# Kernel tuning notes

Hardware: AMD Instinct MI355X
Metric: run time of the kernel (lower is better)

## Reference

```python
import jax, jax.numpy as jnp
import numpy as np

V, E, P, NL, H, I = 50304, 512, 320, 6, 8, 1024
B, S = 2, 1024
HD = P // H            # head_dim = 40
ROT = int(HD * 0.25)   # rotary dims = 10


def layer_norm(x, w, b, eps=1e-5):
    m = jnp.mean(x, -1, keepdims=True)
    v = jnp.mean((x - m) ** 2, -1, keepdims=True)
    return (x - m) * jax.lax.rsqrt(v + eps) * w + b


def setup_inputs() -> dict:
    key = jax.random.key(0)
    ks = jax.random.split(key, 16)
    n = lambda k, s: jax.random.normal(k, s, dtype=jnp.float32) * 0.02
    return dict(
        input_ids=jax.random.randint(ks[0], (B, S), 0, V),
        embed_w=n(ks[1], (V, E)),
        embed_norm_w=jnp.ones((E,)), embed_norm_b=jnp.zeros((E,)),
        dproj_w=n(ks[2], (P + E, P)), dproj_b=jnp.zeros((P,)),
        dproj_ln_w=jnp.ones((P,)), dproj_ln_b=jnp.zeros((P,)),
        ln1_w=jnp.ones((NL, P)), ln1_b=jnp.zeros((NL, P)),
        ln2_w=jnp.ones((NL, P)), ln2_b=jnp.zeros((NL, P)),
        qkv_w=n(ks[3], (NL, P, 3 * P)), qkv_b=jnp.zeros((NL, 3 * P)),
        dense_w=n(ks[4], (NL, P, P)), dense_b=jnp.zeros((NL, P)),
        fc1_w=n(ks[5], (NL, P, I)), fc1_b=jnp.zeros((NL, I)),
        fc2_w=n(ks[6], (NL, I, P)), fc2_b=jnp.zeros((NL, P)),
        final_ln_w=jnp.ones((P,)), final_ln_b=jnp.zeros((P,)),
        lm_head_w=n(ks[7], (V, P)),
    )


def _forward(input_ids, embed_w, embed_norm_w, embed_norm_b, dproj_w, dproj_b,
             dproj_ln_w, dproj_ln_b, ln1_w, ln1_b, ln2_w, ln2_b, qkv_w, qkv_b,
             dense_w, dense_b, fc1_w, fc1_b, fc2_w, fc2_b, final_ln_w, final_ln_b,
             lm_head_w):
    b, s = input_ids.shape
    # 1-2) token embedding + LayerNorm
    te = layer_norm(embed_w[input_ids], embed_norm_w, embed_norm_b)  # [B,S,E]

    # 3) sequential DiverseProjection recurrence over seq_len (lax.scan)
    def step(prev, emb_t):  # prev [B,P], emb_t [B,E]
        h = jnp.concatenate([prev, emb_t], -1) @ dproj_w + dproj_b
        h = jnp.tanh(layer_norm(h, dproj_ln_w, dproj_ln_b))
        return h, h
    _, hs = jax.lax.scan(step, jnp.zeros((b, P), te.dtype), jnp.swapaxes(te, 0, 1))
    x = jnp.swapaxes(hs, 0, 1)  # [B,S,P]

    # RoPE tables (GPT-NeoX style, rotary_pct = 0.25 of head_dim)
    half = ROT // 2
    inv = 1.0 / (10000.0 ** (jnp.arange(0, ROT, 2, dtype=jnp.float32) / ROT))
    freqs = jnp.arange(s, dtype=jnp.float32)[:, None] * inv[None, :]  # [S, ROT/2]
    cos = jnp.cos(jnp.concatenate([freqs, freqs], -1))  # [S, ROT]
    sin = jnp.sin(jnp.concatenate([freqs, freqs], -1))

    def rope(t):  # t: [B,H,S,ROT]
        t1, t2 = t[..., :half], t[..., half:]
        return t * cos + jnp.concatenate([-t2, t1], -1) * sin

    mask = jnp.tril(jnp.ones((s, s), dtype=bool))
    scale = 1.0 / np.sqrt(HD)
    # 4) Pythia (GPT-NeoX) layers: parallel residual attn + mlp
    for l in range(NL):
        a_in = layer_norm(x, ln1_w[l], ln1_b[l])
        qkv = (a_in @ qkv_w[l] + qkv_b[l]).reshape(b, s, H, 3 * HD)
        q, k, v = (jnp.swapaxes(t, 1, 2) for t in jnp.split(qkv, 3, axis=-1))  # [B,H,S,HD]
        q = jnp.concatenate([rope(q[..., :ROT]), q[..., ROT:]], -1)
        k = jnp.concatenate([rope(k[..., :ROT]), k[..., ROT:]], -1)
        scores = jnp.einsum('bhqd,bhkd->bhqk', q, k) * scale
        attn = jax.nn.softmax(jnp.where(mask, scores, jnp.float32(-1e9)), axis=-1)
        ctx = jnp.einsum('bhqk,bhkd->bhqd', attn, v)
        attn_out = jnp.swapaxes(ctx, 1, 2).reshape(b, s, P) @ dense_w[l] + dense_b[l]
        m_in = layer_norm(x, ln2_w[l], ln2_b[l])
        mlp_out = jax.nn.gelu(m_in @ fc1_w[l] + fc1_b[l]) @ fc2_w[l] + fc2_b[l]
        x = x + attn_out + mlp_out
    # 5-6) final LN + LM head (no bias)
    x = layer_norm(x, final_ln_w, final_ln_b)
    return x @ lm_head_w.T  # [B,S,V]


def reference(input_ids, embed_w, embed_norm_w, embed_norm_b, dproj_w, dproj_b,
              dproj_ln_w, dproj_ln_b, ln1_w, ln1_b, ln2_w, ln2_b, qkv_w, qkv_b,
              dense_w, dense_b, fc1_w, fc1_b, fc2_w, fc2_b, final_ln_w, final_ln_b,
              lm_head_w):
    return _forward(input_ids, embed_w, embed_norm_w, embed_norm_b, dproj_w, dproj_b,
                    dproj_ln_w, dproj_ln_b, ln1_w, ln1_b, ln2_w, ln2_b, qkv_w, qkv_b,
                    dense_w, dense_b, fc1_w, fc1_b, fc2_w, fc2_b, final_ln_w,
                    final_ln_b, lm_head_w)
```

## Files before the change

### kernel.cpp

```cpp
#include <hip/hip_runtime.h>

#define VV 50304
#define EE 512
#define PP 320
#define NL 6
#define NH 8
#define II 1024
#define BB 2
#define SS 1024
#define HDD 40

typedef __attribute__((ext_vector_type(8))) __bf16 bf16x8;
typedef __attribute__((ext_vector_type(4))) float f32x4;

__device__ __forceinline__ float gelu_tanh(float x) {
    float x3 = x * x * x;
    return 0.5f * x * (1.f + tanhf(0.7978845608028654f * (x + 0.044715f * x3)));
}

__global__ __launch_bounds__(64) void embed_ln_kernel(
    const int* __restrict__ ids, const float* __restrict__ embed,
    const float* __restrict__ w, const float* __restrict__ b, float* __restrict__ out)
{
    int r = blockIdx.x;
    int lane = threadIdx.x;
    long id = ids[r];
    const float* xr = embed + id * (long)EE;
    float vals[8];
    float s = 0.f;
#pragma unroll
    for (int i = 0; i < 8; ++i) { vals[i] = xr[lane + i * 64]; s += vals[i]; }
#pragma unroll
    for (int m = 32; m >= 1; m >>= 1) s += __shfl_xor(s, m);
    float mean = s * (1.f / 512.f);
    float v = 0.f;
#pragma unroll
    for (int i = 0; i < 8; ++i) { float d = vals[i] - mean; v += d * d; }
#pragma unroll
    for (int m = 32; m >= 1; m >>= 1) v += __shfl_xor(v, m);
    float rstd = rsqrtf(v * (1.f / 512.f) + 1e-5f);
    float* orow = out + (long)r * EE;
#pragma unroll
    for (int i = 0; i < 8; ++i) {
        int c = lane + i * 64;
        orow[c] = (vals[i] - mean) * rstd * w[c] + b[c];
    }
}

__global__ __launch_bounds__(64) void ln_kernel(
    const float* __restrict__ x, const float* __restrict__ w,
    const float* __restrict__ b, float* __restrict__ out, int N)
{
    int r = blockIdx.x, lane = threadIdx.x;
    const float* xr = x + (long)r * N;
    float s = 0.f;
    for (int i = lane; i < N; i += 64) s += xr[i];
#pragma unroll
    for (int m = 32; m >= 1; m >>= 1) s += __shfl_xor(s, m);
    float mean = s / (float)N;
    float v = 0.f;
    for (int i = lane; i < N; i += 64) { float d = xr[i] - mean; v += d * d; }
#pragma unroll
    for (int m = 32; m >= 1; m >>= 1) v += __shfl_xor(v, m);
    float rstd = rsqrtf(v / (float)N + 1e-5f);
    float* orow = out + (long)r * N;
    for (int i = lane; i < N; i += 64) orow[i] = (xr[i] - mean) * rstd * w[i] + b[i];
}

__global__ __launch_bounds__(256) void gemm_kernel(
    const float* __restrict__ A, const float* __restrict__ B,
    const float* __restrict__ bias, float* __restrict__ C,
    int M, int N, int K, int BT, int act,
    const float* __restrict__ add1, const float* __restrict__ add2)
{
    __shared__ __align__(16) __bf16 As[64 * 40];
    __shared__ __align__(16) __bf16 Bs[64 * 40];
    int tid  = threadIdx.x;
    int lane = tid & 63;
    int wv   = tid >> 6;
    int l15  = lane & 15, quad = lane >> 4;
    int bm = blockIdx.y * 64, bn = blockIdx.x * 64;
    int wm = (wv >> 1) * 32, wn = (wv & 1) * 32;
    f32x4 acc[2][2] = {};

    int sm = tid >> 2;
    int sk = (tid & 3) * 8;
    int bk_n = tid & 63;
    int bk_k = (tid >> 6) * 8;

    for (int k0 = 0; k0 < K; k0 += 32) {
        {
            const float* ap = A + (long)(bm + sm) * K + k0 + sk;
            float4 a0 = *(const float4*)ap;
            float4 a1 = *(const float4*)(ap + 4);
            bf16x8 av;
            av[0] = (__bf16)a0.x; av[1] = (__bf16)a0.y; av[2] = (__bf16)a0.z; av[3] = (__bf16)a0.w;
            av[4] = (__bf16)a1.x; av[5] = (__bf16)a1.y; av[6] = (__bf16)a1.z; av[7] = (__bf16)a1.w;
            *(bf16x8*)&As[sm * 40 + sk] = av;
        }
        if (BT == 0) {
            const float* bp = B + (long)(k0 + bk_k) * N + bn + bk_n;
            bf16x8 bv;
#pragma unroll
            for (int i = 0; i < 8; ++i) bv[i] = (__bf16)bp[(long)i * N];
            *(bf16x8*)&Bs[bk_n * 40 + bk_k] = bv;
        } else {
            const float* bp = B + (long)(bn + sm) * K + k0 + sk;
            float4 b0 = *(const float4*)bp;
            float4 b1 = *(const float4*)(bp + 4);
            bf16x8 bv;
            bv[0] = (__bf16)b0.x; bv[1] = (__bf16)b0.y; bv[2] = (__bf16)b0.z; bv[3] = (__bf16)b0.w;
            bv[4] = (__bf16)b1.x; bv[5] = (__bf16)b1.y; bv[6] = (__bf16)b1.z; bv[7] = (__bf16)b1.w;
            *(bf16x8*)&Bs[sm * 40 + sk] = bv;
        }
        __syncthreads();
#pragma unroll
        for (int mt = 0; mt < 2; ++mt) {
            bf16x8 af = *(const bf16x8*)&As[(wm + mt * 16 + l15) * 40 + quad * 8];
#pragma unroll
            for (int nt = 0; nt < 2; ++nt) {
                bf16x8 bfr = *(const bf16x8*)&Bs[(wn + nt * 16 + l15) * 40 + quad * 8];
                acc[mt][nt] = __builtin_amdgcn_mfma_f32_16x16x32_bf16(af, bfr, acc[mt][nt], 0, 0, 0);
            }
        }
        __syncthreads();
    }
#pragma unroll
    for (int mt = 0; mt < 2; ++mt)
#pragma unroll
    for (int nt = 0; nt < 2; ++nt)
#pragma unroll
    for (int r = 0; r < 4; ++r) {
        int grow = bm + wm + mt * 16 + quad * 4 + r;
        int gcol = bn + wn + nt * 16 + l15;
        float v = acc[mt][nt][r];
        if (bias) v += bias[gcol];
        if (act == 1) v = gelu_tanh(v);
        long idx = (long)grow * N + gcol;
        if (add1) v += add1[idx];
        if (add2) v += add2[idx];
        C[idx] = v;
    }
}

__global__ __launch_bounds__(640) void scan_kernel(
    const float* __restrict__ Wtop,
    const float* __restrict__ c,
    const float* __restrict__ lnw, const float* __restrict__ lnb,
    float* __restrict__ x)
{
    __shared__ __align__(16) __bf16 hA[16 * 328];
    __shared__ float yb[2][PP];
    __shared__ float red[24];

    int tid = threadIdx.x;
    int lane = tid & 63;
    int w = tid >> 6;
    int l15 = lane & 15, quad = lane >> 4;

    for (int i = tid; i < 16 * 328; i += 640) hA[i] = (__bf16)0.f;

    bf16x8 bw[2][10];
#pragma unroll
    for (int nt = 0; nt < 2; ++nt) {
        int nn = (w * 2 + nt) * 16 + l15;
#pragma unroll
        for (int kt = 0; kt < 10; ++kt) {
#pragma unroll
            for (int j = 0; j < 8; ++j) {
                int kk = kt * 32 + quad * 8 + j;
                bw[nt][kt][j] = (__bf16)Wtop[(long)kk * PP + nn];
            }
        }
    }

    int sb = tid / PP;
    int jj = tid % PP;
    float lw = lnw[jj], lb = lnb[jj];
    __syncthreads();

    for (int t = 0; t < SS; ++t) {
        float cv = c[((long)sb * SS + t) * PP + jj];
        f32x4 acc0 = {0.f, 0.f, 0.f, 0.f}, acc1 = {0.f, 0.f, 0.f, 0.f};
#pragma unroll
        for (int kt = 0; kt < 10; ++kt) {
            bf16x8 a = *(const bf16x8*)&hA[l15 * 328 + kt * 32 + quad * 8];
            acc0 = __builtin_amdgcn_mfma_f32_16x16x32_bf16(a, bw[0][kt], acc0, 0, 0, 0);
            acc1 = __builtin_amdgcn_mfma_f32_16x16x32_bf16(a, bw[1][kt], acc1, 0, 0, 0);
        }
        if (quad == 0) {
            yb[0][(w * 2 + 0) * 16 + l15] = acc0[0];
            yb[1][(w * 2 + 0) * 16 + l15] = acc0[1];
            yb[0][(w * 2 + 1) * 16 + l15] = acc1[0];
            yb[1][(w * 2 + 1) * 16 + l15] = acc1[1];
        }
        __syncthreads();
        float yv = yb[sb][jj] + cv;
        float s1 = yv, s2 = yv * yv;
#pragma unroll
        for (int m = 32; m >= 1; m >>= 1) { s1 += __shfl_xor(s1, m); s2 += __shfl_xor(s2, m); }
        if (lane == 0) { red[w * 2] = s1; red[w * 2 + 1] = s2; }
        __syncthreads();
        float S1 = 0.f, S2 = 0.f;
        int wbase = sb * 5;
#pragma unroll
        for (int i = 0; i < 5; ++i) { S1 += red[(wbase + i) * 2]; S2 += red[(wbase + i) * 2 + 1]; }
        float mean = S1 * (1.f / (float)PP);
        float var  = S2 * (1.f / (float)PP) - mean * mean;
        float h = tanhf((yv - mean) * rsqrtf(var + 1e-5f) * lw + lb);
        x[((long)sb * SS + t) * PP + jj] = h;
        hA[sb * 328 + jj] = (__bf16)h;
        __syncthreads();
    }
}

__global__ __launch_bounds__(256) void rope_kernel(float* __restrict__ qkv)
{
    int t = blockIdx.x * 256 + threadIdx.x;
    if (t >= BB * SS * NH) return;
    int h = t & 7;
    int s = (t >> 3) & (SS - 1);
    int b = t >> 13;
    float* p = qkv + ((long)(b * SS + s)) * 960 + h * 120;
    const float inv[5] = {1.f, 0.158489319f, 0.0251188643f, 0.00398107171f, 0.000630957344f};
    float* q = p;
    float* k = p + HDD;
#pragma unroll
    for (int i = 0; i < 5; ++i) {
        float ang = (float)s * inv[i];
        float sn, cs;
        sincosf(ang, &sn, &cs);
        float q1 = q[i], q2 = q[i + 5];
        q[i]     = q1 * cs - q2 * sn;
        q[i + 5] = q2 * cs + q1 * sn;
        float k1 = k[i], k2 = k[i + 5];
        k[i]     = k1 * cs - k2 * sn;
        k[i + 5] = k2 * cs + k1 * sn;
    }
}

__global__ __launch_bounds__(256) void attn_kernel(
    const float* __restrict__ qkv, float* __restrict__ ctx)
{
    int qt = blockIdx.x & 15;
    int h  = (blockIdx.x >> 4) & 7;
    int b  = blockIdx.x >> 7;
    int tid = threadIdx.x;
    __shared__ float Qs[64][41], Ks[64][41], Vs[64][41];
    __shared__ float Ss[64][65];
    __shared__ float mS[64], lS[64], aS[64];
    const float scale = 0.15811388300841897f;
    long base = (long)b * SS * 960 + h * 120;
    int q0 = qt * 64;

    for (int i = tid; i < 64 * HDD; i += 256) {
        int r = i / HDD, d = i % HDD;
        Qs[r][d] = qkv[base + (long)(q0 + r) * 960 + d] * scale;
    }
    if (tid < 64) { mS[tid] = -1e30f; lS[tid] = 0.f; }
    float O[10];
#pragma unroll
    for (int i = 0; i < 10; ++i) O[i] = 0.f;
    int qo = tid >> 2, dg = (tid & 3) * 10;
    int sq = tid >> 2, sk16 = (tid & 3) * 16;
    __syncthreads();

    for (int kt = 0; kt <= qt; ++kt) {
        int k0 = kt * 64;
        for (int i = tid; i < 64 * HDD; i += 256) {
            int r = i / HDD, d = i % HDD;
            Ks[r][d] = qkv[base + (long)(k0 + r) * 960 + HDD + d];
            Vs[r][d] = qkv[base + (long)(k0 + r) * 960 + 2 * HDD + d];
        }
        __syncthreads();
#pragma unroll 1
        for (int kk = 0; kk < 16; ++kk) {
            int kcol = sk16 + kk;
            float s = 0.f;
#pragma unroll
            for (int d = 0; d < HDD; ++d) s += Qs[sq][d] * Ks[kcol][d];
            if (k0 + kcol > q0 + sq) s = -1e9f;
            Ss[sq][kcol] = s;
        }
        __syncthreads();
        if (tid < 64) {
            float mOld = mS[tid];
            float mNew = mOld;
            for (int j = 0; j < 64; ++j) mNew = fmaxf(mNew, Ss[tid][j]);
            float alpha = __expf(mOld - mNew);
            float psum = 0.f;
            for (int j = 0; j < 64; ++j) {
                float p = __expf(Ss[tid][j] - mNew);
                Ss[tid][j] = p;
                psum += p;
            }
            lS[tid] = lS[tid] * alpha + psum;
            mS[tid] = mNew;
            aS[tid] = alpha;
        }
        __syncthreads();
        float alpha = aS[qo];
#pragma unroll
        for (int i = 0; i < 10; ++i) O[i] *= alpha;
        for (int k = 0; k < 64; ++k) {
            float p = Ss[qo][k];
#pragma unroll
            for (int i = 0; i < 10; ++i) O[i] += p * Vs[k][dg + i];
        }
        __syncthreads();
    }
    float linv = 1.f / lS[qo];
#pragma unroll
    for (int i = 0; i < 10; ++i)
        ctx[((long)(b * SS + q0 + qo)) * PP + h * HDD + dg + i] = O[i] * linv;
}

extern "C" void kernel_launch(void* const* d_in, const int* in_sizes, int n_in,
                              void* d_out, int out_size, void* d_ws, size_t ws_size,
                              hipStream_t stream)
{
    (void)in_sizes; (void)n_in; (void)out_size; (void)ws_size;
    const int*   ids       = (const int*)d_in[0];
    const float* embed_w   = (const float*)d_in[1];
    const float* embed_nw  = (const float*)d_in[2];
    const float* embed_nb  = (const float*)d_in[3];
    const float* dproj_w   = (const float*)d_in[4];
    const float* dproj_b   = (const float*)d_in[5];
    const float* dproj_lnw = (const float*)d_in[6];
    const float* dproj_lnb = (const float*)d_in[7];
    const float* ln1_w     = (const float*)d_in[8];
    const float* ln1_b     = (const float*)d_in[9];
    const float* ln2_w     = (const float*)d_in[10];
    const float* ln2_b     = (const float*)d_in[11];
    const float* qkv_w     = (const float*)d_in[12];
    const float* qkv_b     = (const float*)d_in[13];
    const float* dense_w   = (const float*)d_in[14];
    const float* dense_b   = (const float*)d_in[15];
    const float* fc1_w     = (const float*)d_in[16];
    const float* fc1_b     = (const float*)d_in[17];
    const float* fc2_w     = (const float*)d_in[18];
    const float* fc2_b     = (const float*)d_in[19];
    const float* fln_w     = (const float*)d_in[20];
    const float* fln_b     = (const float*)d_in[21];
    const float* lm_w      = (const float*)d_in[22];
    float* out = (float*)d_out;
    float* ws  = (float*)d_ws;

    const long R = (long)BB * SS;
    float* te    = ws;
    float* cbuf  = te   + 1048576;
    float* x     = cbuf + 655360;
    float* lnbuf = x    + 655360;
    float* qkv   = lnbuf + 655360;
    float* ctx   = qkv  + 1966080;
    float* attn  = ctx  + 655360;
    float* mlp1  = attn + 655360;

    embed_ln_kernel<<<R, 64, 0, stream>>>(ids, embed_w, embed_nw, embed_nb, te);
    gemm_kernel<<<dim3(PP / 64, R / 64), 256, 0, stream>>>(
        te, dproj_w + (long)PP * PP, dproj_b, cbuf, R, PP, EE, 0, 0, nullptr, nullptr);
    scan_kernel<<<1, 640, 0, stream>>>(dproj_w, cbuf, dproj_lnw, dproj_lnb, x);

    for (int l = 0; l < NL; ++l) {
        ln_kernel<<<R, 64, 0, stream>>>(x, ln1_w + l * PP, ln1_b + l * PP, lnbuf, PP);
        gemm_kernel<<<dim3(960 / 64, R / 64), 256, 0, stream>>>(
            lnbuf, qkv_w + (long)l * PP * 960, qkv_b + l * 960, qkv, R, 960, PP, 0, 0, nullptr, nullptr);
        rope_kernel<<<(BB * SS * NH + 255) / 256, 256, 0, stream>>>(qkv);
        attn_kernel<<<BB * NH * 16, 256, 0, stream>>>(qkv, ctx);
        gemm_kernel<<<dim3(PP / 64, R / 64), 256, 0, stream>>>(
            ctx, dense_w + (long)l * PP * PP, dense_b + l * PP, attn, R, PP, PP, 0, 0, nullptr, nullptr);
        ln_kernel<<<R, 64, 0, stream>>>(x, ln2_w + l * PP, ln2_b + l * PP, lnbuf, PP);
        gemm_kernel<<<dim3(II / 64, R / 64), 256, 0, stream>>>(
            lnbuf, fc1_w + (long)l * PP * II, fc1_b + l * II, mlp1, R, II, PP, 0, 1, nullptr, nullptr);
        gemm_kernel<<<dim3(PP / 64, R / 64), 256, 0, stream>>>(
            mlp1, fc2_w + (long)l * II * PP, fc2_b + l * PP, x, R, PP, II, 0, 0, x, attn);
    }
    ln_kernel<<<R, 64, 0, stream>>>(x, fln_w, fln_b, lnbuf, PP);
    gemm_kernel<<<dim3(VV / 64, R / 64), 256, 0, stream>>>(
        lnbuf, lm_w, nullptr, out, R, VV, PP, 1, 0, nullptr, nullptr);
}
```

Before: 4.395 ms.

## Restructure sequential scan kernel to 4 waves with DPP reductions and prefetch

Rewrites the sequential projection scan so one block of 4 waves runs it instead of 10, and each wave computes 5 column tiles with MFMA. The per-row LayerNorm statistics are reduced with DPP within 16-lane groups and combined across waves through a small shared array, removing one of the three barriers per timestep. The next step's c values are prefetched into registers, and tanhf is replaced by an exp-based formula with clamping. Fewer waves mean fewer MFMAs in parallel per step and more register pressure from holding 50 weight fragments per lane.

```diff
diff --git a/kernel.cpp b/kernel.cpp
--- a/kernel.cpp
+++ b/kernel.cpp
@@ -17,6 +17,18 @@
     float x3 = x * x * x;
     return 0.5f * x * (1.f + tanhf(0.7978845608028654f * (x + 0.044715f * x3)));
 }
+
+template<int CTRL>
+__device__ __forceinline__ float dpp_reduce_add(float v) {
+    int s = __builtin_amdgcn_update_dpp(0, __builtin_bit_cast(int, v), CTRL, 0xF, 0xF, true);
+    return v + __builtin_bit_cast(float, s);
+}
+#define DPPRED16(x) do { \
+    x = dpp_reduce_add<0xB1>(x);   \
+    x = dpp_reduce_add<0x4E>(x);   \
+    x = dpp_reduce_add<0x141>(x);  \
+    x = dpp_reduce_add<0x140>(x);  \
+} while (0)
 
 __global__ __launch_bounds__(64) void embed_ln_kernel(
     const int* __restrict__ ids, const float* __restrict__ embed,
@@ -143,27 +155,27 @@
     }
 }
 
-__global__ __launch_bounds__(640) void scan_kernel(
+__global__ __launch_bounds__(256, 1) void scan_kernel(
     const float* __restrict__ Wtop,
     const float* __restrict__ c,
     const float* __restrict__ lnw, const float* __restrict__ lnb,
     float* __restrict__ x)
 {
     __shared__ __align__(16) __bf16 hA[16 * 328];
-    __shared__ float yb[2][PP];
-    __shared__ float red[24];
+    __shared__ __align__(16) float yb2[PP * 2];
+    __shared__ __align__(16) float red[16];
 
     int tid = threadIdx.x;
     int lane = tid & 63;
     int w = tid >> 6;
     int l15 = lane & 15, quad = lane >> 4;
 
-    for (int i = tid; i < 16 * 328; i += 640) hA[i] = (__bf16)0.f;
-
-    bf16x8 bw[2][10];
-#pragma unroll
-    for (int nt = 0; nt < 2; ++nt) {
-        int nn = (w * 2 + nt) * 16 + l15;
+    for (int i = tid; i < 16 * 328; i += 256) hA[i] = (__bf16)0.f;
+
+    bf16x8 bw[5][10];
+#pragma unroll
+    for (int nt = 0; nt < 5; ++nt) {
+        int nn = w * 80 + nt * 16 + l15;
 #pragma unroll
         for (int kt = 0; kt < 10; ++kt) {
 #pragma unroll
@@ -174,42 +186,98 @@
         }
     }
 
-    int sb = tid / PP;
-    int jj = tid % PP;
-    float lw = lnw[jj], lb = lnb[jj];
+    int nv = (tid < 128) ? 3 : 2;
+    int vb[3], vcol[3];
+    vb[0] = 0;            vcol[0] = tid;
+    vb[1] = (tid >= 64);  vcol[1] = vb[1] ? (tid - 64) : (tid + 256);
+    vb[2] = 1;            vcol[2] = tid + 192;
+    float lwv[3], lbv[3];
+    long xbase[3]; int ybo[3], hao[3];
+#pragma unroll
+    for (int i = 0; i < 3; ++i) {
+        if (i < nv) {
+            lwv[i] = lnw[vcol[i]]; lbv[i] = lnb[vcol[i]];
+            xbase[i] = (long)vb[i] * SS * PP + vcol[i];
+            ybo[i] = vcol[i] * 2 + vb[i];
+            hao[i] = vb[i] * 328 + vcol[i];
+        }
+    }
+
+    int ccol = w * 80 + l15;
+    const float* cp0 = c + ccol;
+    const float* cp1 = c + (long)SS * PP + ccol;
+    float cc0[5], cc1[5];
+#pragma unroll
+    for (int nt = 0; nt < 5; ++nt) { cc0[nt] = cp0[nt * 16]; cc1[nt] = cp1[nt * 16]; }
     __syncthreads();
 
     for (int t = 0; t < SS; ++t) {
-        float cv = c[((long)sb * SS + t) * PP + jj];
-        f32x4 acc0 = {0.f, 0.f, 0.f, 0.f}, acc1 = {0.f, 0.f, 0.f, 0.f};
+        int tn = (t + 1 < SS) ? (t + 1) : t;
+        float nc0[5], nc1[5];
+#pragma unroll
+        for (int nt = 0; nt < 5; ++nt) {
+            nc0[nt] = cp0[(long)tn * PP + nt * 16];
+            nc1[nt] = cp1[(long)tn * PP + nt * 16];
+        }
+
+        f32x4 acc[5] = {};
 #pragma unroll
         for (int kt = 0; kt < 10; ++kt) {
             bf16x8 a = *(const bf16x8*)&hA[l15 * 328 + kt * 32 + quad * 8];
-            acc0 = __builtin_amdgcn_mfma_f32_16x16x32_bf16(a, bw[0][kt], acc0, 0, 0, 0);
-            acc1 = __builtin_amdgcn_mfma_f32_16x16x32_bf16(a, bw[1][kt], acc1, 0, 0, 0);
-        }
+#pragma unroll
+            for (int nt = 0; nt < 5; ++nt)
+                acc[nt] = __builtin_amdgcn_mfma_f32_16x16x32_bf16(a, bw[nt][kt], acc[nt], 0, 0, 0);
+        }
+
+        float ya[5], yc[5];
+#pragma unroll
+        for (int nt = 0; nt < 5; ++nt) { ya[nt] = acc[nt][0] + cc0[nt]; yc[nt] = acc[nt][1] + cc1[nt]; }
+        float s10 = ya[0] + ya[1] + ya[2] + ya[3] + ya[4];
+        float s20 = ya[0]*ya[0] + ya[1]*ya[1] + ya[2]*ya[2] + ya[3]*ya[3] + ya[4]*ya[4];
+        float s11 = yc[0] + yc[1] + yc[2] + yc[3] + yc[4];
+        float s21 = yc[0]*yc[0] + yc[1]*yc[1] + yc[2]*yc[2] + yc[3]*yc[3] + yc[4]*yc[4];
+        DPPRED16(s10); DPPRED16(s20); DPPRED16(s11); DPPRED16(s21);
         if (quad == 0) {
-            yb[0][(w * 2 + 0) * 16 + l15] = acc0[0];
-            yb[1][(w * 2 + 0) * 16 + l15] = acc0[1];
-            yb[0][(w * 2 + 1) * 16 + l15] = acc1[0];
-            yb[1][(w * 2 + 1) * 16 + l15] = acc1[1];
-        }
-        __syncthreads();
-        float yv = yb[sb][jj] + cv;
-        float s1 = yv, s2 = yv * yv;
-#pragma unroll
-        for (int m = 32; m >= 1; m >>= 1) { s1 += __shfl_xor(s1, m); s2 += __shfl_xor(s2, m); }
-        if (lane == 0) { red[w * 2] = s1; red[w * 2 + 1] = s2; }
-        __syncthreads();
-        float S1 = 0.f, S2 = 0.f;
-        int wbase = sb * 5;
-#pragma unroll
-        for (int i = 0; i < 5; ++i) { S1 += red[(wbase + i) * 2]; S2 += red[(wbase + i) * 2 + 1]; }
-        float mean = S1 * (1.f / (float)PP);
-        float var  = S2 * (1.f / (float)PP) - mean * mean;
-        float h = tanhf((yv - mean) * rsqrtf(var + 1e-5f) * lw + lb);
-        x[((long)sb * SS + t) * PP + jj] = h;
-        hA[sb * 328 + jj] = (__bf16)h;
+#pragma unroll
+            for (int nt = 0; nt < 5; ++nt) {
+                float2 p; p.x = ya[nt]; p.y = yc[nt];
+                *(float2*)&yb2[(w * 80 + nt * 16 + l15) * 2] = p;
+            }
+        }
+        if (lane == 0) {
+            f32x4 r; r[0] = s10; r[1] = s20; r[2] = s11; r[3] = s21;
+            *(f32x4*)&red[w * 4] = r;
+        }
+        __syncthreads();
+
+        f32x4 r0 = *(const f32x4*)&red[0];
+        f32x4 r1 = *(const f32x4*)&red[4];
+        f32x4 r2 = *(const f32x4*)&red[8];
+        f32x4 r3 = *(const f32x4*)&red[12];
+        float S10 = r0[0] + r1[0] + r2[0] + r3[0];
+        float S20 = r0[1] + r1[1] + r2[1] + r3[1];
+        float S11 = r0[2] + r1[2] + r2[2] + r3[2];
+        float S21 = r0[3] + r1[3] + r2[3] + r3[3];
+        float mean0 = S10 * (1.f / 320.f), mean1 = S11 * (1.f / 320.f);
+        float rstd0 = rsqrtf(S20 * (1.f / 320.f) - mean0 * mean0 + 1e-5f);
+        float rstd1 = rsqrtf(S21 * (1.f / 320.f) - mean1 * mean1 + 1e-5f);
+
+#pragma unroll
+        for (int i = 0; i < 3; ++i) {
+            if (i < nv) {
+                float y = yb2[ybo[i]];
+                float m  = vb[i] ? mean1 : mean0;
+                float rs = vb[i] ? rstd1 : rstd0;
+                float z = (y - m) * rs * lwv[i] + lbv[i];
+                z = fminf(fmaxf(z, -15.f), 15.f);
+                float e = __expf(2.f * z);
+                float h = (e - 1.f) / (e + 1.f);
+                x[xbase[i] + (long)t * PP] = h;
+                hA[hao[i]] = (__bf16)h;
+            }
+        }
+#pragma unroll
+        for (int nt = 0; nt < 5; ++nt) { cc0[nt] = nc0[nt]; cc1[nt] = nc1[nt]; }
         __syncthreads();
     }
 }
@@ -359,7 +427,7 @@
     embed_ln_kernel<<<R, 64, 0, stream>>>(ids, embed_w, embed_nw, embed_nb, te);
     gemm_kernel<<<dim3(PP / 64, R / 64), 256, 0, stream>>>(
         te, dproj_w + (long)PP * PP, dproj_b, cbuf, R, PP, EE, 0, 0, nullptr, nullptr);
-    scan_kernel<<<1, 640, 0, stream>>>(dproj_w, cbuf, dproj_lnw, dproj_lnb, x);
+    scan_kernel<<<1, 256, 0, stream>>>(dproj_w, cbuf, dproj_lnw, dproj_lnb, x);
 
     for (int l = 0; l < NL; ++l) {
         ln_kernel<<<R, 64, 0, stream>>>(x, ln1_w + l * PP, ln1_b + l * PP, lnbuf, PP);
```

After: 4.312 ms. Within noise of the previous version (-1.9%).
